# Kernel optimization log

Hardware: AMD Instinct MI355X
Metric: run time of the kernel (lower is better)

Reference implementation:

```python
import jax, jax.numpy as jnp
import numpy as np

N_NODES = 10000
N_EDGES = 640000
D_IN = 128
D_OUT = 128


def setup_inputs() -> dict:
    key = jax.random.key(0)
    k_x, k_val, k_w, k_row, k_col = jax.random.split(key, 5)
    # Glorot init for weight, zeros for bias (matches _weight_init)
    limit = float(np.sqrt(6.0 / (D_IN + D_OUT)))
    weight = jax.random.uniform(k_w, (D_IN, D_OUT), jnp.float32, -limit, limit)
    return {
        "x": jax.random.normal(k_x, (N_NODES, D_IN), jnp.float32),
        "adj_val": jax.random.uniform(k_val, (N_EDGES,), jnp.float32),  # normalized edge weights of sparse adj
        "weight": weight,
        "bias": jnp.zeros((D_OUT,), jnp.float32),
        "adj_row": jax.random.randint(k_row, (N_EDGES,), 0, N_NODES, jnp.int32),
        "adj_col": jax.random.randint(k_col, (N_EDGES,), 0, N_NODES, jnp.int32),
    }


def reference(x, adj_val, weight, bias, adj_row, adj_col):
    # dense GEMM: h = x @ W  -> [N, D_OUT]
    h = jnp.matmul(x, weight)
    # SpMM with COO adjacency: out[r] = sum_{e: row[e]=r} val[e] * h[col[e]]
    msg = adj_val[:, None] * h[adj_col]  # [E, D_OUT] gather + scale
    out = jax.ops.segment_sum(msg, adj_row, num_segments=x.shape[0])
    return out + bias
```

## Files before the change

kernel.cpp:

```cpp
#include <hip/hip_runtime.h>

#define N_NODES 10000
#define N_EDGES 640000
#define D 128

#define GEMM_BLOCKS 157
#define TOT_BLOCKS 256
#define CAP 32
#define OVF_CAP 8192
#define LSTR 136

typedef unsigned int uint32;
typedef unsigned short u16;
using short8 = __attribute__((ext_vector_type(8))) short;
using f32x4  = __attribute__((ext_vector_type(4))) float;

__device__ __forceinline__ uint32 f2bf_bits(float f) {
    uint32 u = __float_as_uint(f);
    return (u + 0x7FFFu + ((u >> 16) & 1u)) >> 16;
}
__device__ __forceinline__ uint32 pack2(float lo, float hi) {
    return f2bf_bits(lo) | (f2bf_bits(hi) << 16);
}

__device__ __forceinline__ void scat_one(int r, uint32 rc, int s,
                                         int* __restrict__ cursor,
                                         uint32* __restrict__ region,
                                         int* ovf_cnt, uint2* ovf)
{
    int pos = atomicAdd(&cursor[s * N_NODES + r], 1);
    if (pos < CAP) {
        region[(r * 8 + s) * CAP + pos] = rc;
    } else {
        int o = atomicAdd(ovf_cnt, 1);
        if (o < OVF_CAP) ovf[o] = make_uint2((uint32)r, rc);
    }
}

__global__ __launch_bounds__(256) void gemm_scatter_kernel(
    const float* __restrict__ x, const float* __restrict__ w,
    const int* __restrict__ row, const int* __restrict__ col,
    const float* __restrict__ val,
    uint32* __restrict__ h2, int* __restrict__ cursor,
    int* __restrict__ ovf_cnt, uint2* __restrict__ ovf,
    uint32* __restrict__ region)
{
    const int t = threadIdx.x;

    if (blockIdx.x < GEMM_BLOCKS) {
        __shared__ u16 Xs[64 * LSTR];
        __shared__ u16 Ws[128 * LSTR];

        #pragma unroll
        for (int i = 0; i < 8; ++i) {
            int lin = t + i * 256;
            int rw  = lin >> 5;
            int f4  = lin & 31;
            int gr = blockIdx.x * 64 + rw;
            if (gr >= N_NODES) gr = N_NODES - 1;
            float4 xv = *(const float4*)&x[(size_t)gr * D + f4 * 4];
            *(uint2*)&Xs[rw * LSTR + f4 * 4] =
                make_uint2(pack2(xv.x, xv.y), pack2(xv.z, xv.w));
        }
        #pragma unroll
        for (int i = 0; i < 32; ++i) {
            int lin = t + i * 256;
            int c = lin & 127;
            int m = lin >> 7;
            float w0 = w[(2 * m) * D + c];
            float w1 = w[(2 * m + 1) * D + c];
            *(uint32*)&Ws[c * LSTR + 2 * m] = pack2(w0, w1);
        }
        __syncthreads();

        const int wv = t >> 6, lane = t & 63;
        const int q = lane >> 4, cl = lane & 15;
        f32x4 acc[8] = {};
        const u16* arow = &Xs[(wv * 16 + cl) * LSTR];
        #pragma unroll
        for (int k0 = 0; k0 < D; k0 += 32) {
            short8 af = *(const short8*)&arow[k0 + q * 8];
            #pragma unroll
            for (int ct = 0; ct < 8; ++ct) {
                short8 bf = *(const short8*)&Ws[(ct * 16 + cl) * LSTR + k0 + q * 8];
                acc[ct] = __builtin_amdgcn_mfma_f32_16x16x32_bf16(af, bf, acc[ct], 0, 0, 0);
            }
        }
        #pragma unroll
        for (int reg = 0; reg < 4; ++reg) {
            int node = blockIdx.x * 64 + wv * 16 + q * 4 + reg;
            if (node < N_NODES) {
                uint32* base = h2 + (size_t)node * 64 + cl;
                #pragma unroll
                for (int ct = 0; ct < 4; ++ct)
                    base[ct * 16] = pack2(acc[ct][reg], acc[ct + 4][reg]);
            }
        }
    }

    {
        const int xcc = blockIdx.x & 7;
        const int tid    = blockIdx.x * 256 + t;
        const int stride = TOT_BLOCKS * 256;
        const int4*   row4 = (const int4*)row;
        const int4*   col4 = (const int4*)col;
        const float4* val4 = (const float4*)val;
        for (int i = tid; i < N_EDGES / 4; i += stride) {
            int4 r = row4[i]; int4 c = col4[i]; float4 v = val4[i];
            scat_one(r.x, (uint32)c.x | (f2bf_bits(v.x) << 16), xcc, cursor, region, ovf_cnt, ovf);
            scat_one(r.y, (uint32)c.y | (f2bf_bits(v.y) << 16), xcc, cursor, region, ovf_cnt, ovf);
            scat_one(r.z, (uint32)c.z | (f2bf_bits(v.z) << 16), xcc, cursor, region, ovf_cnt, ovf);
            scat_one(r.w, (uint32)c.w | (f2bf_bits(v.w) << 16), xcc, cursor, region, ovf_cnt, ovf);
        }
    }
}

__global__ __launch_bounds__(256) void spmm_kernel(
    const uint32* __restrict__ region, const int* __restrict__ cursor,
    const int* __restrict__ ovf_cnt, const uint2* __restrict__ ovf,
    const uint32* __restrict__ h2, const float* __restrict__ bias,
    float* __restrict__ out)
{
    const int t = threadIdx.x;
    const int lane = t & 63;
    const int r = blockIdx.x * 4 + (t >> 6);

    uint32 rl[4];
    #pragma unroll
    for (int i = 0; i < 4; ++i)
        rl[i] = region[r * 256 + i * 64 + lane];
    int ns[8];
    #pragma unroll
    for (int s = 0; s < 8; ++s) {
        int c = cursor[s * N_NODES + r];
        ns[s] = (c < CAP) ? c : CAP;
    }

    float a0 = 0.f, a1 = 0.f;
    #pragma unroll
    for (int s = 0; s < 8; ++s) {
        const int v    = (int)rl[s >> 1];
        const int half = (s & 1) * 32;
        const int n    = ns[s];
        int j = 0;
        for (; j + 4 <= n; j += 4) {
            uint32 q0 = (uint32)__builtin_amdgcn_readlane(v, half + j);
            uint32 q1 = (uint32)__builtin_amdgcn_readlane(v, half + j + 1);
            uint32 q2 = (uint32)__builtin_amdgcn_readlane(v, half + j + 2);
            uint32 q3 = (uint32)__builtin_amdgcn_readlane(v, half + j + 3);
            uint32 h0 = h2[((q0 & 0xFFFFu) << 6) + lane];
            uint32 h1 = h2[((q1 & 0xFFFFu) << 6) + lane];
            uint32 h2v = h2[((q2 & 0xFFFFu) << 6) + lane];
            uint32 h3 = h2[((q3 & 0xFFFFu) << 6) + lane];
            a0 = fmaf(__uint_as_float(q0 & 0xFFFF0000u), __uint_as_float(h0 << 16), a0);
            a1 = fmaf(__uint_as_float(q0 & 0xFFFF0000u), __uint_as_float(h0 & 0xFFFF0000u), a1);
            a0 = fmaf(__uint_as_float(q1 & 0xFFFF0000u), __uint_as_float(h1 << 16), a0);
            a1 = fmaf(__uint_as_float(q1 & 0xFFFF0000u), __uint_as_float(h1 & 0xFFFF0000u), a1);
            a0 = fmaf(__uint_as_float(q2 & 0xFFFF0000u), __uint_as_float(h2v << 16), a0);
            a1 = fmaf(__uint_as_float(q2 & 0xFFFF0000u), __uint_as_float(h2v & 0xFFFF0000u), a1);
            a0 = fmaf(__uint_as_float(q3 & 0xFFFF0000u), __uint_as_float(h3 << 16), a0);
            a1 = fmaf(__uint_as_float(q3 & 0xFFFF0000u), __uint_as_float(h3 & 0xFFFF0000u), a1);
        }
        for (; j < n; ++j) {
            uint32 q0 = (uint32)__builtin_amdgcn_readlane(v, half + j);
            uint32 h0 = h2[((q0 & 0xFFFFu) << 6) + lane];
            a0 = fmaf(__uint_as_float(q0 & 0xFFFF0000u), __uint_as_float(h0 << 16), a0);
            a1 = fmaf(__uint_as_float(q0 & 0xFFFF0000u), __uint_as_float(h0 & 0xFFFF0000u), a1);
        }
    }

    int novf = ovf_cnt[0];
    if (novf > OVF_CAP) novf = OVF_CAP;
    for (int k = 0; k < novf; ++k) {
        uint2 e = ovf[k];
        if (e.x == (uint32)r) {
            uint32 qq = e.y;
            uint32 hv = h2[((qq & 0xFFFFu) << 6) + lane];
            a0 = fmaf(__uint_as_float(qq & 0xFFFF0000u), __uint_as_float(hv << 16), a0);
            a1 = fmaf(__uint_as_float(qq & 0xFFFF0000u), __uint_as_float(hv & 0xFFFF0000u), a1);
        }
    }

    out[(size_t)r * D + lane]      = a0 + bias[lane];
    out[(size_t)r * D + 64 + lane] = a1 + bias[lane + 64];
}

extern "C" void kernel_launch(void* const* d_in, const int* in_sizes, int n_in,
                              void* d_out, int out_size, void* d_ws, size_t ws_size,
                              hipStream_t stream)
{
    const float* x    = (const float*)d_in[0];
    const float* aval = (const float*)d_in[1];
    const float* w    = (const float*)d_in[2];
    const float* bias = (const float*)d_in[3];
    const int* arow   = (const int*)d_in[4];
    const int* acol   = (const int*)d_in[5];

    char* ws = (char*)d_ws;
    uint32* h2     = (uint32*)(ws);
    int*    cursor = (int*)(ws + 2560000);
    int*    ovfcnt = (int*)(ws + 2880000);
    uint2*  ovf    = (uint2*)(ws + 2880064);
    uint32* region = (uint32*)(ws + 2945600);

    hipMemsetAsync(ws + 2560000, 0, 320004, stream);

    gemm_scatter_kernel<<<TOT_BLOCKS, 256, 0, stream>>>(
        x, w, arow, acol, aval, h2, cursor, ovfcnt, ovf, region);
    spmm_kernel<<<N_NODES / 4, 256, 0, stream>>>(
        region, cursor, ovfcnt, ovf, h2, bias, (float*)d_out);
}
```

Measured before the change: 120.0 us.

## Compact per-row edge lists in LDS and software-pipeline gathers eight deep

The SpMM kernel packs each row's eight per-XCC edge slots into one contiguous LDS list using a prefix sum. It then runs a single loop over that list with an eight-deep rotating prefetch of h2 rows, replacing the per-slot readlane loops with their short tails. The goal is more memory-level parallelism and less loop overhead per row. In exchange it adds LDS traffic, pads the list with zero entries that cost extra gathers of node 0, and uses a plain waitcnt instead of a barrier. It also reads up to eight entries past the padded end, which may touch neighbouring wave buffers or slots that were never written.

After: 115.0 us. 1.04x faster.

```diff
diff --git a/kernel.cpp b/kernel.cpp
--- a/kernel.cpp
+++ b/kernel.cpp
@@ -9,6 +9,7 @@
 #define CAP 32
 #define OVF_CAP 8192
 #define LSTR 136
+#define QPAD 272
 
 typedef unsigned int uint32;
 typedef unsigned short u16;
@@ -121,53 +122,74 @@
     const uint32* __restrict__ h2, const float* __restrict__ bias,
     float* __restrict__ out)
 {
+    __shared__ uint32 qbuf[4 * QPAD];
     const int t = threadIdx.x;
     const int lane = t & 63;
-    const int r = blockIdx.x * 4 + (t >> 6);
+    const int wid  = t >> 6;
+    const int r = blockIdx.x * 4 + wid;
+    uint32* qb = &qbuf[wid * QPAD];
 
     uint32 rl[4];
     #pragma unroll
     for (int i = 0; i < 4; ++i)
         rl[i] = region[r * 256 + i * 64 + lane];
-    int ns[8];
+
+    int ns[8], pref[9];
+    pref[0] = 0;
     #pragma unroll
     for (int s = 0; s < 8; ++s) {
         int c = cursor[s * N_NODES + r];
         ns[s] = (c < CAP) ? c : CAP;
-    }
-
+        pref[s + 1] = pref[s] + ns[s];
+    }
+    const int ntot = pref[8];
+
+    #pragma unroll
+    for (int i = 0; i < 4; ++i) {
+        int p  = lane & 31;
+        int hi = lane >> 5;
+        int n_  = hi ? ns[2 * i + 1]   : ns[2 * i];
+        int pf  = hi ? pref[2 * i + 1] : pref[2 * i];
+        if (p < n_) qb[pf + p] = rl[i];
+    }
+    if (lane < 16) qb[ntot + lane] = 0;
+    __builtin_amdgcn_s_waitcnt(0);
+
+    const int npad = (ntot + 7) & ~7;
     float a0 = 0.f, a1 = 0.f;
-    #pragma unroll
-    for (int s = 0; s < 8; ++s) {
-        const int v    = (int)rl[s >> 1];
-        const int half = (s & 1) * 32;
-        const int n    = ns[s];
-        int j = 0;
-        for (; j + 4 <= n; j += 4) {
-            uint32 q0 = (uint32)__builtin_amdgcn_readlane(v, half + j);
-            uint32 q1 = (uint32)__builtin_amdgcn_readlane(v, half + j + 1);
-            uint32 q2 = (uint32)__builtin_amdgcn_readlane(v, half + j + 2);
-            uint32 q3 = (uint32)__builtin_amdgcn_readlane(v, half + j + 3);
-            uint32 h0 = h2[((q0 & 0xFFFFu) << 6) + lane];
-            uint32 h1 = h2[((q1 & 0xFFFFu) << 6) + lane];
-            uint32 h2v = h2[((q2 & 0xFFFFu) << 6) + lane];
-            uint32 h3 = h2[((q3 & 0xFFFFu) << 6) + lane];
-            a0 = fmaf(__uint_as_float(q0 & 0xFFFF0000u), __uint_as_float(h0 << 16), a0);
-            a1 = fmaf(__uint_as_float(q0 & 0xFFFF0000u), __uint_as_float(h0 & 0xFFFF0000u), a1);
-            a0 = fmaf(__uint_as_float(q1 & 0xFFFF0000u), __uint_as_float(h1 << 16), a0);
-            a1 = fmaf(__uint_as_float(q1 & 0xFFFF0000u), __uint_as_float(h1 & 0xFFFF0000u), a1);
-            a0 = fmaf(__uint_as_float(q2 & 0xFFFF0000u), __uint_as_float(h2v << 16), a0);
-            a1 = fmaf(__uint_as_float(q2 & 0xFFFF0000u), __uint_as_float(h2v & 0xFFFF0000u), a1);
-            a0 = fmaf(__uint_as_float(q3 & 0xFFFF0000u), __uint_as_float(h3 << 16), a0);
-            a1 = fmaf(__uint_as_float(q3 & 0xFFFF0000u), __uint_as_float(h3 & 0xFFFF0000u), a1);
-        }
-        for (; j < n; ++j) {
-            uint32 q0 = (uint32)__builtin_amdgcn_readlane(v, half + j);
-            uint32 h0 = h2[((q0 & 0xFFFFu) << 6) + lane];
-            a0 = fmaf(__uint_as_float(q0 & 0xFFFF0000u), __uint_as_float(h0 << 16), a0);
-            a1 = fmaf(__uint_as_float(q0 & 0xFFFF0000u), __uint_as_float(h0 & 0xFFFF0000u), a1);
-        }
-    }
+
+    uint32 rq0,rq1,rq2,rq3,rq4,rq5,rq6,rq7;
+    uint32 hh0,hh1,hh2,hh3,hh4,hh5,hh6,hh7;
+    rq0 = qb[0]; hh0 = h2[((rq0 & 0xFFFFu) << 6) + lane];
+    rq1 = qb[1]; hh1 = h2[((rq1 & 0xFFFFu) << 6) + lane];
+    rq2 = qb[2]; hh2 = h2[((rq2 & 0xFFFFu) << 6) + lane];
+    rq3 = qb[3]; hh3 = h2[((rq3 & 0xFFFFu) << 6) + lane];
+    rq4 = qb[4]; hh4 = h2[((rq4 & 0xFFFFu) << 6) + lane];
+    rq5 = qb[5]; hh5 = h2[((rq5 & 0xFFFFu) << 6) + lane];
+    rq6 = qb[6]; hh6 = h2[((rq6 & 0xFFFFu) << 6) + lane];
+    rq7 = qb[7]; hh7 = h2[((rq7 & 0xFFFFu) << 6) + lane];
+
+#define CONSUME_PREFETCH(RQ, HH, P)                                          \
+    {                                                                        \
+        a0 = fmaf(__uint_as_float(RQ & 0xFFFF0000u),                         \
+                  __uint_as_float(HH << 16), a0);                            \
+        a1 = fmaf(__uint_as_float(RQ & 0xFFFF0000u),                         \
+                  __uint_as_float(HH & 0xFFFF0000u), a1);                    \
+        uint32 rn = qb[j + 8 + P];                                           \
+        RQ = rn; HH = h2[((rn & 0xFFFFu) << 6) + lane];                      \
+    }
+
+    for (int j = 0; j < npad; j += 8) {
+        CONSUME_PREFETCH(rq0, hh0, 0)
+        CONSUME_PREFETCH(rq1, hh1, 1)
+        CONSUME_PREFETCH(rq2, hh2, 2)
+        CONSUME_PREFETCH(rq3, hh3, 3)
+        CONSUME_PREFETCH(rq4, hh4, 4)
+        CONSUME_PREFETCH(rq5, hh5, 5)
+        CONSUME_PREFETCH(rq6, hh6, 6)
+        CONSUME_PREFETCH(rq7, hh7, 7)
+    }
+#undef CONSUME_PREFETCH
 
     int novf = ovf_cnt[0];
     if (novf > OVF_CAP) novf = OVF_CAP;
```
